# Kernel tuning notes

Measured on AMD Instinct MI355X. Metric: run time of the kernel, lower is better.

Reference implementation:

```python
import jax, jax.numpy as jnp
import numpy as np
import math
from jax import lax

B, T, GS = 16, 511, 1
OBS, OUT = 60, 30
D, H, L = 1024, 16, 8
DFF, HID = 4096, 100
S = T + GS
DH = D // H
EPS = 1e-5


def _ln(x, g, b):
    m = jnp.mean(x, axis=-1, keepdims=True)
    v = jnp.mean(jnp.square(x - m), axis=-1, keepdims=True)
    return (x - m) * lax.rsqrt(v + EPS) * g + b


def setup_inputs():
    key = jax.random.key(0)
    ks = iter(jax.random.split(key, 32))
    def n(shape):
        return jax.random.normal(next(ks), shape, dtype=jnp.float32) * 0.02
    return {
        "states": jax.random.normal(next(ks), (B, T, OBS), dtype=jnp.float32),
        "goals": jax.random.normal(next(ks), (B, GS, OBS), dtype=jnp.float32),
        "Wtok": n((OBS, D)), "btok": jnp.zeros((D,), jnp.float32),
        "pos": n((1, S, D)),
        "ln1_g": jnp.ones((L, D), jnp.float32), "ln1_b": jnp.zeros((L, D), jnp.float32),
        "Wq": n((L, D, D)), "bq": jnp.zeros((L, D), jnp.float32),
        "Wk": n((L, D, D)), "bk": jnp.zeros((L, D), jnp.float32),
        "Wv": n((L, D, D)), "bv": jnp.zeros((L, D), jnp.float32),
        "Wp": n((L, D, D)), "bp": jnp.zeros((L, D), jnp.float32),
        "ln2_g": jnp.ones((L, D), jnp.float32), "ln2_b": jnp.zeros((L, D), jnp.float32),
        "Wm1": n((L, D, DFF)), "bm1": jnp.zeros((L, DFF), jnp.float32),
        "Wm2": n((L, DFF, D)), "bm2": jnp.zeros((L, D), jnp.float32),
        "lnf_g": jnp.ones((D,), jnp.float32), "lnf_b": jnp.zeros((D,), jnp.float32),
        "Wh1": n((D, HID)), "bh1": jnp.zeros((HID,), jnp.float32),
        "Wh2": n((HID, OUT)), "bh2": jnp.zeros((OUT,), jnp.float32),
    }


def reference(states, goals, Wtok, btok, pos, ln1_g, ln1_b, Wq, bq, Wk, bk, Wv, bv, Wp, bp,
              ln2_g, ln2_b, Wm1, bm1, Wm2, bm2, lnf_g, lnf_b, Wh1, bh1, Wh2, bh2):
    # token + positional embeddings (dropout is identity in eval mode, pdrop=0)
    goal_x = goals @ Wtok + btok + pos[:, :GS]
    state_x = states @ Wtok + btok + pos[:, GS:S]
    x = jnp.concatenate([goal_x, state_x], axis=1)  # (B, S, D)
    mask = jnp.tril(jnp.ones((S, S), dtype=bool))
    scale = 1.0 / math.sqrt(DH)

    def block(x, p):
        g1, b1, wq, bq_, wk, bk_, wv, bv_, wp, bp_, g2, b2, w1, bm1_, w2, bm2_ = p
        h = _ln(x, g1, b1)
        q = (h @ wq + bq_).reshape(B, S, H, DH).transpose(0, 2, 1, 3)  # (B,H,S,DH)
        k = (h @ wk + bk_).reshape(B, S, H, DH).transpose(0, 2, 1, 3)
        v = (h @ wv + bv_).reshape(B, S, H, DH).transpose(0, 2, 1, 3)
        att = jnp.einsum('bhqd,bhkd->bhqk', q, k) * scale
        att = jnp.where(mask, att, -jnp.inf)
        att = jax.nn.softmax(att, axis=-1)
        y = jnp.einsum('bhqk,bhkd->bhqd', att, v)
        y = y.transpose(0, 2, 1, 3).reshape(B, S, D) @ wp + bp_
        x = x + y
        h = _ln(x, g2, b2)
        x = x + (jax.nn.gelu(h @ w1 + bm1_, approximate=False) @ w2 + bm2_)
        return x, None

    x, _ = lax.scan(block, x, (ln1_g, ln1_b, Wq, bq, Wk, bk, Wv, bv, Wp, bp,
                               ln2_g, ln2_b, Wm1, bm1, Wm2, bm2))
    x = _ln(x, lnf_g, lnf_b)[:, GS:]  # drop goal tokens -> (B, T, D)
    h = jax.nn.silu(x @ Wh1 + bh1)
    return h @ Wh2 + bh2
```

## Files before the change

kernel.cpp:

```cpp
#include <hip/hip_runtime.h>
#include <cstdint>
#include <math.h>

#define NB_B   16
#define NB_T   511
#define NB_S   512
#define NB_OBS 60
#define NB_D   1024
#define NB_H   16
#define NB_L   8
#define NB_DFF 4096
#define NB_HID 100
#define NB_OUT 30
#define NB_M   8192
#define QKV_S  3072

typedef __attribute__((ext_vector_type(8))) short  short8;
typedef __attribute__((ext_vector_type(4))) short  short4v;
typedef __attribute__((ext_vector_type(4))) float  f32x4;
typedef __attribute__((ext_vector_type(8))) __bf16 bf16x8;

template <int N_> struct ic { static constexpr int v = N_; };

__device__ __forceinline__ short f2bf(float f) {
  union { float f; unsigned u; } a; a.f = f;
  unsigned u = a.u + 0x7fffu + ((a.u >> 16) & 1u);
  return (short)(u >> 16);
}

__device__ __forceinline__ void load_lds16(const void* g, void* l) {
  __builtin_amdgcn_global_load_lds(
      (__attribute__((address_space(1))) unsigned int*)(uintptr_t)g,
      (__attribute__((address_space(3))) unsigned int*)(unsigned)(uintptr_t)l,
      16, 0, 0);
}

__device__ __forceinline__ f32x4 mfma16(short8 a, short8 b, f32x4 c) {
  return __builtin_amdgcn_mfma_f32_16x16x32_bf16(
      __builtin_bit_cast(bf16x8, a), __builtin_bit_cast(bf16x8, b), c, 0, 0, 0);
}

__device__ __forceinline__ float gelu_fast(float v) {
  const float t = 1.5957691216057308f * (v + 0.044715f * v * v * v);
  const float e = __expf(fminf(t, 30.f));
  return v * (e / (e + 1.f));
}

__global__ __launch_bounds__(256) void tconv2_kernel(
    const float* __restrict__ src, short* __restrict__ dst,
    int R, int C, size_t sstride, size_t dstride) {
  __shared__ float t[64][65];
  const float* s0 = src + blockIdx.z * sstride;
  short* d0 = dst + blockIdx.z * dstride;
  const int c0 = blockIdx.x * 64, r0 = blockIdx.y * 64;
#pragma unroll
  for (int i = 0; i < 4; i++) {
    const int idx = threadIdx.x + i * 256;
    const int r = idx >> 4, c4 = (idx & 15) * 4;
    const float4 v = *(const float4*)&s0[(size_t)(r0 + r) * C + c0 + c4];
    t[r][c4 + 0] = v.x; t[r][c4 + 1] = v.y; t[r][c4 + 2] = v.z; t[r][c4 + 3] = v.w;
  }
  __syncthreads();
#pragma unroll
  for (int i = 0; i < 2; i++) {
    const int idx = threadIdx.x + i * 256;
    const int c = idx >> 3, g = (idx & 7) * 8;
    short8 o;
#pragma unroll
    for (int j = 0; j < 8; j++) o[j] = f2bf(t[g + j][c]);
    *(short8*)&d0[(size_t)(c0 + c) * R + r0 + g] = o;
  }
}

__global__ __launch_bounds__(256) void whead_prep(
    const float* __restrict__ Wh1, const float* __restrict__ bh1,
    short* __restrict__ Wh1t, float* __restrict__ bh1p) {
  const int idx = blockIdx.x * 256 + threadIdx.x;
  const int n = idx >> 10, k = idx & 1023;
  Wh1t[idx] = (n < NB_HID) ? f2bf(Wh1[k * NB_HID + n]) : (short)0;
  if (idx < 128) bh1p[idx] = (idx < NB_HID) ? bh1[idx] : 0.f;
}

__global__ __launch_bounds__(256) void qkvbias_prep(
    const float* __restrict__ bq, const float* __restrict__ bk,
    const float* __restrict__ bv, float* __restrict__ outb) {
  const int idx = blockIdx.x * 256 + threadIdx.x;
  const int l = idx / QKV_S, r = idx - l * QKV_S;
  const int z = r >> 10, c = r & 1023;
  const float* src = (z == 0) ? bq : ((z == 1) ? bk : bv);
  outb[idx] = src[l * NB_D + c];
}

__global__ __launch_bounds__(256) void embed2_kernel(
    const float* __restrict__ states, const float* __restrict__ goals,
    const float* __restrict__ Wtok, const float* __restrict__ btok,
    const float* __restrict__ pos, float* __restrict__ x) {
  const int r0 = blockIdx.x * 8;
  __shared__ float tok[8][NB_OBS];
  for (int idx = threadIdx.x; idx < 8 * NB_OBS; idx += 256) {
    const int r = idx / NB_OBS, o = idx - r * NB_OBS;
    const int row = r0 + r, b = row >> 9, s = row & 511;
    tok[r][o] = (s == 0) ? goals[b * NB_OBS + o]
                         : states[((size_t)b * NB_T + (s - 1)) * NB_OBS + o];
  }
  __syncthreads();
#pragma unroll
  for (int i = 0; i < 4; i++) {
    const int d = threadIdx.x + i * 256;
    float acc[8];
#pragma unroll
    for (int r = 0; r < 8; r++) acc[r] = 0.f;
    for (int o = 0; o < NB_OBS; o++) {
      const float wv = Wtok[o * NB_D + d];
#pragma unroll
      for (int r = 0; r < 8; r++) acc[r] += tok[r][o] * wv;
    }
    const float bt = btok[d];
#pragma unroll
    for (int r = 0; r < 8; r++) {
      const int row = r0 + r, s = row & 511;
      x[(size_t)row * NB_D + d] = acc[r] + bt + pos[(size_t)s * NB_D + d];
    }
  }
}

template <typename OutT>
__global__ __launch_bounds__(256) void ln_wave(
    const float* __restrict__ xin, const float* __restrict__ gam,
    const float* __restrict__ bet, OutT* __restrict__ outp) {
  const int row = blockIdx.x * 4 + (threadIdx.x >> 6);
  const int lane = threadIdx.x & 63;
  const float4* src = (const float4*)(xin + (size_t)row * NB_D);
  float4 v[4];
  float s = 0.f, s2 = 0.f;
#pragma unroll
  for (int i = 0; i < 4; i++) {
    v[i] = src[lane + 64 * i];
    s += v[i].x + v[i].y + v[i].z + v[i].w;
    s2 += v[i].x * v[i].x + v[i].y * v[i].y + v[i].z * v[i].z + v[i].w * v[i].w;
  }
#pragma unroll
  for (int o = 32; o; o >>= 1) {
    s += __shfl_xor(s, o, 64);
    s2 += __shfl_xor(s2, o, 64);
  }
  const float mean = s * (1.f / NB_D);
  const float var = s2 * (1.f / NB_D) - mean * mean;
  const float rs = rsqrtf(var + 1e-5f);
#pragma unroll
  for (int i = 0; i < 4; i++) {
    const float4 g4 = ((const float4*)gam)[lane + 64 * i];
    const float4 b4 = ((const float4*)bet)[lane + 64 * i];
    const float o0 = (v[i].x - mean) * rs * g4.x + b4.x;
    const float o1 = (v[i].y - mean) * rs * g4.y + b4.y;
    const float o2 = (v[i].z - mean) * rs * g4.z + b4.z;
    const float o3 = (v[i].w - mean) * rs * g4.w + b4.w;
    if constexpr (sizeof(OutT) == 2) {
      short4v r = {f2bf(o0), f2bf(o1), f2bf(o2), f2bf(o3)};
      *(short4v*)((short*)outp + (size_t)row * NB_D + (lane + 64 * i) * 4) = r;
    } else {
      ((float4*)((float*)outp + (size_t)row * NB_D))[lane + 64 * i] =
          make_float4(o0, o1, o2, o3);
    }
  }
}

template <int ACT, bool RESID, typename OutT>
__global__ __launch_bounds__(256) void gemm_bt(
    const short* __restrict__ A, const short* __restrict__ Bt,
    const float* __restrict__ bias, const float* __restrict__ resid,
    OutT* __restrict__ C, int N, int K) {
  __shared__ short As[128][32];
  __shared__ short Bs[128][32];
  const int bm = blockIdx.y * 128, bn = blockIdx.x * 128;
  const int tid = threadIdx.x;
  const int w = tid >> 6, lane = tid & 63;
  const int wr = (w >> 1) * 64, wc = (w & 1) * 64;
  const int rr = lane & 15, sg = lane >> 4;

  f32x4 acc[4][4];
#pragma unroll
  for (int i = 0; i < 4; i++)
#pragma unroll
    for (int j = 0; j < 4; j++) acc[i][j] = f32x4{0.f, 0.f, 0.f, 0.f};

  const int srow0 = w * 32 + (lane >> 2);
  const int sslot = lane & 3;

  for (int k0 = 0; k0 < K; k0 += 32) {
    __syncthreads();
#pragma unroll
    for (int inst = 0; inst < 2; inst++) {
      const int r = srow0 + inst * 16;
      const int sl = sslot ^ ((r >> 1) & 3);
      load_lds16(A + (size_t)(bm + r) * K + k0 + sl * 8, &As[w * 32 + inst * 16][0]);
      load_lds16(Bt + (size_t)(bn + r) * K + k0 + sl * 8, &Bs[w * 32 + inst * 16][0]);
    }
    __syncthreads();
    short8 a[4], b[4];
#pragma unroll
    for (int i = 0; i < 4; i++) {
      const int r = wr + i * 16 + rr;
      a[i] = *(const short8*)&As[r][(sg ^ ((r >> 1) & 3)) * 8];
      const int c = wc + i * 16 + rr;
      b[i] = *(const short8*)&Bs[c][(sg ^ ((c >> 1) & 3)) * 8];
    }
#pragma unroll
    for (int i = 0; i < 4; i++)
#pragma unroll
      for (int j = 0; j < 4; j++) acc[i][j] = mfma16(a[i], b[j], acc[i][j]);
  }

#pragma unroll
  for (int j = 0; j < 4; j++) {
    const int col = bn + wc + j * 16 + rr;
    const float bv = bias[col];
#pragma unroll
    for (int i = 0; i < 4; i++) {
#pragma unroll
      for (int q = 0; q < 4; q++) {
        const int row = bm + wr + i * 16 + sg * 4 + q;
        float v = acc[i][j][q] + bv;
        if constexpr (RESID) v += resid[(size_t)row * N + col];
        if constexpr (ACT == 1) v = gelu_fast(v);
        if constexpr (ACT == 2) v = v / (1.f + __expf(-v));
        if constexpr (sizeof(OutT) == 2) C[(size_t)row * N + col] = (OutT)f2bf(v);
        else C[(size_t)row * N + col] = v;
      }
    }
  }
}

template <int BM, int N, int K, int ACT, bool RESID, typename OutT>
__device__ __forceinline__ void gemmv4_core(
    const short* __restrict__ A, const short* __restrict__ Bt,
    const float* __restrict__ bias, const float* __restrict__ resid,
    OutT* __restrict__ C) {
  constexpr int MI = BM / 32;
  constexpr int NK = K / 32;
  constexpr int NBN = N / 128;
  constexpr int NWG = (NB_M / BM) * NBN;
  constexpr int QC = NWG / 8;
  constexpr int L = 2 + BM / 64;
  constexpr int SA = BM * 32;

  __shared__ short As[3][SA];
  __shared__ short Bs[3][128 * 32];

  int wg = blockIdx.x;
  wg = (wg & 7) * QC + (wg >> 3);
  const int bm = (wg / NBN) * BM;
  const int bn = (wg % NBN) * 128;

  const int tid = threadIdx.x;
  const int w = tid >> 6, lane = tid & 63;
  const int wm = w >> 1, wn = w & 1;
  const int rr = lane & 15, sg = lane >> 4;
  const int lrow = lane >> 2, lslot = lane & 3;
  const int sslot = lslot ^ ((lrow >> 1) & 3);

  const short* Asrc = A + (size_t)(bm + w * 16 + lrow) * K + sslot * 8;
  const short* Bsrc = Bt + (size_t)(bn + w * 16 + lrow) * K + sslot * 8;
  short* Adst = &As[0][w * 512];
  short* Bdst = &Bs[0][w * 512];

  const int ar = wm * (BM / 2) + rr;
  const int br = wn * 64 + rr;
  const int aoff = ar * 32 + ((sg ^ ((ar >> 1) & 3)) * 8);
  const int boff = br * 32 + ((sg ^ ((br >> 1) & 3)) * 8);

  f32x4 acc[MI][4];
#pragma unroll
  for (int i = 0; i < MI; i++)
#pragma unroll
    for (int j = 0; j < 4; j++) acc[i][j] = f32x4{0.f, 0.f, 0.f, 0.f};

  auto stage = [&](int sb, int k0) {
    load_lds16(Bsrc + k0,                  Bdst + sb * 4096);
    load_lds16(Bsrc + (size_t)64 * K + k0, Bdst + sb * 4096 + 2048);
#pragma unroll
    for (int c = 0; c < BM / 64; c++)
      load_lds16(Asrc + (size_t)(c * 64) * K + k0, Adst + sb * SA + c * 2048);
  };

  auto gate = [&]() {
    if constexpr (L == 6) asm volatile("s_waitcnt vmcnt(6)" ::: "memory");
    else                  asm volatile("s_waitcnt vmcnt(4)" ::: "memory");
  };

  stage(0, 0);
  stage(1, 32);
  gate();
  __builtin_amdgcn_s_barrier();

  auto ktile = [&](auto BUFC, auto SBUFC, int t) {
    constexpr int BUF = decltype(BUFC)::v;
    constexpr int SBUF = decltype(SBUFC)::v;
    const short* Ab = &As[BUF][0];
    const short* Bb = &Bs[BUF][0];
    if (t + 2 < NK) stage(SBUF, (t + 2) * 32);
    short8 a[MI], b[4];
#pragma unroll
    for (int i = 0; i < MI; i++) a[i] = *(const short8*)(Ab + aoff + i * 512);
#pragma unroll
    for (int j = 0; j < 4; j++) b[j] = *(const short8*)(Bb + boff + j * 512);
    __builtin_amdgcn_s_setprio(1);
#pragma unroll
    for (int i = 0; i < MI; i++)
#pragma unroll
      for (int j = 0; j < 4; j++) acc[i][j] = mfma16(a[i], b[j], acc[i][j]);
    __builtin_amdgcn_s_setprio(0);
    if (t + 2 < NK)      gate();
    else if (t + 1 < NK) asm volatile("s_waitcnt vmcnt(0)" ::: "memory");
    __builtin_amdgcn_s_barrier();
  };

  int t = 0;
#pragma unroll 1
  for (; t + 3 <= NK; t += 3) {
    ktile(ic<0>{}, ic<2>{}, t);
    ktile(ic<1>{}, ic<0>{}, t + 1);
    ktile(ic<2>{}, ic<1>{}, t + 2);
  }
  if constexpr (NK % 3 >= 1) ktile(ic<0>{}, ic<2>{}, NK - NK % 3);
  if constexpr (NK % 3 >= 2) ktile(ic<1>{}, ic<0>{}, NK - NK % 3 + 1);

  const int col0 = bn + wn * 64 + rr;
  float bv[4];
#pragma unroll
  for (int j = 0; j < 4; j++) bv[j] = bias[col0 + j * 16];
#pragma unroll
  for (int i = 0; i < MI; i++) {
#pragma unroll
    for (int q = 0; q < 4; q++) {
      const size_t row = bm + wm * (BM / 2) + i * 16 + sg * 4 + q;
      float v0 = acc[i][0][q] + bv[0];
      float v1 = acc[i][1][q] + bv[1];
      float v2 = acc[i][2][q] + bv[2];
      float v3 = acc[i][3][q] + bv[3];
      if constexpr (RESID) {
        const float* rrow = resid + row * N + col0;
        v0 += rrow[0]; v1 += rrow[16]; v2 += rrow[32]; v3 += rrow[48];
      }
      if constexpr (ACT == 1) {
        v0 = gelu_fast(v0); v1 = gelu_fast(v1);
        v2 = gelu_fast(v2); v3 = gelu_fast(v3);
      }
      OutT* crow = C + row * N + col0;
      if constexpr (sizeof(OutT) == 2) {
        crow[0] = (OutT)f2bf(v0); crow[16] = (OutT)f2bf(v1);
        crow[32] = (OutT)f2bf(v2); crow[48] = (OutT)f2bf(v3);
      } else {
        crow[0] = v0; crow[16] = v1; crow[32] = v2; crow[48] = v3;
      }
    }
  }
}

template <int BM, int N, int K, int ACT, bool RESID, typename OutT>
__global__ __launch_bounds__(256, 2) void gemmv4(
    const short* __restrict__ A, const short* __restrict__ Bt,
    const float* __restrict__ bias, const float* __restrict__ resid,
    OutT* __restrict__ C) {
  gemmv4_core<BM, N, K, ACT, RESID, OutT>(A, Bt, bias, resid, C);
}

__global__ __launch_bounds__(256) void attn_kernel(
    const short* __restrict__ qkv, short* __restrict__ out) {
  const int qt = blockIdx.x, hh = blockIdx.y, bb = blockIdx.z;
  const int tid = threadIdx.x;
  const int w = tid >> 6, lane = tid & 63;
  const int rr = lane & 15, sg = lane >> 4;

  __shared__ short Ks[64][64];
  __shared__ short Vt[64][64];
  __shared__ short Ps[4][16][64];

  short8 qf[2];
  {
    const size_t qrow = (size_t)bb * NB_S + qt * 64 + w * 16 + rr;
#pragma unroll
    for (int ks = 0; ks < 2; ks++)
      qf[ks] = *(const short8*)&qkv[qrow * QKV_S + hh * 64 + ks * 32 + sg * 8];
  }

  float mrow[4], lrow[4];
  f32x4 o[4];
#pragma unroll
  for (int j = 0; j < 4; j++) { mrow[j] = -INFINITY; lrow[j] = 0.f; }
#pragma unroll
  for (int nb = 0; nb < 4; nb++) o[nb] = f32x4{0.f, 0.f, 0.f, 0.f};

  for (int kt = 0; kt <= qt; kt++) {
    __syncthreads();
    {
      const int p = lane & 7;
#pragma unroll
      for (int inst = 0; inst < 2; inst++) {
        const int r = w * 16 + inst * 8 + (lane >> 3);
        const int sl = p ^ (r & 7);
        load_lds16(qkv + ((size_t)bb * NB_S + kt * 64 + r) * QKV_S + 1024 + hh * 64 + sl * 8,
                   &Ks[w * 16 + inst * 8][0]);
      }
    }
    {
#pragma unroll
      for (int cc = 0; cc < 2; cc++) {
        const int c = tid * 2 + cc;
        const int sk = c >> 3, sl = c & 7;
        short8 vv = *(const short8*)&qkv[((size_t)bb * NB_S + kt * 64 + sk) * QKV_S + 2048 + hh * 64 + sl * 8];
        const int ss = sk >> 3;
#pragma unroll
        for (int j = 0; j < 8; j++) {
          const int dh = sl * 8 + j;
          Vt[dh][(ss ^ (dh & 7)) * 8 + (sk & 7)] = vv[j];
        }
      }
    }
    __syncthreads();

    f32x4 sf[4];
#pragma unroll
    for (int nb = 0; nb < 4; nb++) sf[nb] = f32x4{0.f, 0.f, 0.f, 0.f};
#pragma unroll
    for (int ks = 0; ks < 2; ks++) {
#pragma unroll
      for (int nb = 0; nb < 4; nb++) {
        const int ck = nb * 16 + rr;
        short8 kf = *(const short8*)&Ks[ck][((ks * 4 + sg) ^ (ck & 7)) * 8];
        sf[nb] = mfma16(qf[ks], kf, sf[nb]);
      }
    }
    const int rbase = qt * 64 + w * 16 + sg * 4;
    float pmax[4] = {-INFINITY, -INFINITY, -INFINITY, -INFINITY};
#pragma unroll
    for (int nb = 0; nb < 4; nb++) {
      const int cg = kt * 64 + nb * 16 + rr;
#pragma unroll
      for (int j = 0; j < 4; j++) {
        float sv = sf[nb][j] * 0.125f;
        if (cg > rbase + j) sv = -INFINITY;
        sf[nb][j] = sv;
        pmax[j] = fmaxf(pmax[j], sv);
      }
    }
#pragma unroll
    for (int o1 = 1; o1 < 16; o1 <<= 1)
#pragma unroll
      for (int j = 0; j < 4; j++)
        pmax[j] = fmaxf(pmax[j], __shfl_xor(pmax[j], o1, 64));

    float resc[4], psum[4];
#pragma unroll
    for (int j = 0; j < 4; j++) {
      const float mn = fmaxf(mrow[j], pmax[j]);
      resc[j] = __expf(mrow[j] - mn);
      mrow[j] = mn;
      psum[j] = 0.f;
    }
#pragma unroll
    for (int nb = 0; nb < 4; nb++)
#pragma unroll
      for (int j = 0; j < 4; j++) {
        const float p = __expf(sf[nb][j] - mrow[j]);
        sf[nb][j] = p;
        psum[j] += p;
      }
#pragma unroll
    for (int o1 = 1; o1 < 16; o1 <<= 1)
#pragma unroll
      for (int j = 0; j < 4; j++) psum[j] += __shfl_xor(psum[j], o1, 64);
#pragma unroll
    for (int j = 0; j < 4; j++) lrow[j] = lrow[j] * resc[j] + psum[j];
#pragma unroll
    for (int nb = 0; nb < 4; nb++)
#pragma unroll
      for (int j = 0; j < 4; j++) o[nb][j] *= resc[j];

#pragma unroll
    for (int nb = 0; nb < 4; nb++) {
      const int ck = nb * 16 + rr;
      const int ss = ck >> 3;
#pragma unroll
      for (int j = 0; j < 4; j++) {
        const int rq = sg * 4 + j;
        Ps[w][rq][(ss ^ (rq & 7)) * 8 + (ck & 7)] = f2bf(sf[nb][j]);
      }
    }
#pragma unroll
    for (int ks = 0; ks < 2; ks++) {
      short8 pf = *(const short8*)&Ps[w][rr][((ks * 4 + sg) ^ (rr & 7)) * 8];
#pragma unroll
      for (int nb = 0; nb < 4; nb++) {
        const int dh = nb * 16 + rr;
        short8 vf = *(const short8*)&Vt[dh][((ks * 4 + sg) ^ (dh & 7)) * 8];
        o[nb] = mfma16(pf, vf, o[nb]);
      }
    }
  }

  {
    const size_t orow0 = (size_t)bb * NB_S + qt * 64 + w * 16;
#pragma unroll
    for (int nb = 0; nb < 4; nb++)
#pragma unroll
      for (int j = 0; j < 4; j++) {
        const float v = o[nb][j] / lrow[j];
        out[(orow0 + sg * 4 + j) * NB_D + hh * 64 + nb * 16 + rr] = f2bf(v);
      }
  }
}

__global__ __launch_bounds__(256) void head2_kernel(
    const float* __restrict__ hbuf, const float* __restrict__ Wh2,
    const float* __restrict__ bh2, float* __restrict__ outp) {
  __shared__ float hs[8][NB_HID];
  const int g0 = blockIdx.x * 8;
  for (int idx = threadIdx.x; idx < 8 * NB_HID; idx += 256) {
    const int r = idx / NB_HID, k = idx - r * NB_HID;
    const int gt = g0 + r;
    const int b = gt / NB_T, tt = gt - b * NB_T;
    hs[r][k] = hbuf[(size_t)(b * NB_S + 1 + tt) * 128 + k];
  }
  __syncthreads();
  const int r = threadIdx.x >> 5, c = threadIdx.x & 31;
  if (c < NB_OUT) {
    float acc = bh2[c];
#pragma unroll
    for (int k = 0; k < NB_HID; k++) acc += hs[r][k] * Wh2[k * NB_OUT + c];
    outp[(size_t)(g0 + r) * NB_OUT + c] = acc;
  }
}

extern "C" void kernel_launch(void* const* d_in, const int* in_sizes, int n_in,
                              void* d_out, int out_size, void* d_ws, size_t ws_size,
                              hipStream_t stream) {
  const float* states = (const float*)d_in[0];
  const float* goals  = (const float*)d_in[1];
  const float* Wtok   = (const float*)d_in[2];
  const float* btok   = (const float*)d_in[3];
  const float* pos    = (const float*)d_in[4];
  const float* ln1_g  = (const float*)d_in[5];
  const float* ln1_b  = (const float*)d_in[6];
  const float* Wq     = (const float*)d_in[7];
  const float* bq     = (const float*)d_in[8];
  const float* Wk     = (const float*)d_in[9];
  const float* bk     = (const float*)d_in[10];
  const float* Wv     = (const float*)d_in[11];
  const float* bv     = (const float*)d_in[12];
  const float* Wp     = (const float*)d_in[13];
  const float* bp     = (const float*)d_in[14];
  const float* ln2_g  = (const float*)d_in[15];
  const float* ln2_b  = (const float*)d_in[16];
  const float* Wm1    = (const float*)d_in[17];
  const float* bm1    = (const float*)d_in[18];
  const float* Wm2    = (const float*)d_in[19];
  const float* bm2    = (const float*)d_in[20];
  const float* lnf_g  = (const float*)d_in[21];
  const float* lnf_b  = (const float*)d_in[22];
  const float* Wh1    = (const float*)d_in[23];
  const float* bh1    = (const float*)d_in[24];
  const float* Wh2    = (const float*)d_in[25];
  const float* bh2    = (const float*)d_in[26];

  char* wsp = (char*)d_ws;
  size_t off = 0;
  auto carve = [&](size_t bytes) -> char* {
    char* p = wsp + off;
    off += (bytes + 1023) & ~(size_t)1023;
    return p;
  };
  short* Wqkv_t = (short*)carve((size_t)NB_L * 3 * NB_D * NB_D * 2);
  short* Wp_t   = (short*)carve((size_t)NB_L * NB_D * NB_D * 2);
  short* Wm1_t  = (short*)carve((size_t)NB_L * NB_DFF * NB_D * 2);
  short* Wm2_t  = (short*)carve((size_t)NB_L * NB_D * NB_DFF * 2);
  float* x      = (float*)carve((size_t)NB_M * NB_D * 4);
  short* h      = (short*)carve((size_t)NB_M * NB_D * 2);
  short* qkvb   = (short*)carve((size_t)NB_M * QKV_S * 2);
  short* mlp    = (short*)carve((size_t)NB_M * NB_DFF * 2);
  short* Wh1t   = (short*)carve((size_t)128 * NB_D * 2);
  float* bh1p   = (float*)carve(128 * 4);
  float* bqkv   = (float*)carve((size_t)NB_L * QKV_S * 4);
  short* attout = mlp;
  float* hbuf   = (float*)qkvb;

  const dim3 thr(256);
  const size_t DD = (size_t)NB_D * NB_D;
  const size_t DF = (size_t)NB_D * NB_DFF;

  tconv2_kernel<<<dim3(16, 16, NB_L), thr, 0, stream>>>(Wq, Wqkv_t + 0 * DD, NB_D, NB_D, DD, 3 * DD);
  tconv2_kernel<<<dim3(16, 16, NB_L), thr, 0, stream>>>(Wk, Wqkv_t + 1 * DD, NB_D, NB_D, DD, 3 * DD);
  tconv2_kernel<<<dim3(16, 16, NB_L), thr, 0, stream>>>(Wv, Wqkv_t + 2 * DD, NB_D, NB_D, DD, 3 * DD);
  tconv2_kernel<<<dim3(16, 16, NB_L), thr, 0, stream>>>(Wp, Wp_t, NB_D, NB_D, DD, DD);
  tconv2_kernel<<<dim3(64, 16, NB_L), thr, 0, stream>>>(Wm1, Wm1_t, NB_D, NB_DFF, DF, DF);
  tconv2_kernel<<<dim3(16, 64, NB_L), thr, 0, stream>>>(Wm2, Wm2_t, NB_DFF, NB_D, DF, DF);
  whead_prep<<<512, thr, 0, stream>>>(Wh1, bh1, Wh1t, bh1p);
  qkvbias_prep<<<96, thr, 0, stream>>>(bq, bk, bv, bqkv);

  embed2_kernel<<<NB_M / 8, thr, 0, stream>>>(states, goals, Wtok, btok, pos, x);

  for (int l = 0; l < NB_L; l++) {
    ln_wave<short><<<NB_M / 4, thr, 0, stream>>>(x, ln1_g + l * NB_D, ln1_b + l * NB_D, h);
    gemmv4<256, QKV_S, NB_D, 0, false, short><<<768, thr, 0, stream>>>(
        h, Wqkv_t + (size_t)l * 3 * DD, bqkv + (size_t)l * QKV_S, nullptr, qkvb);
    attn_kernel<<<dim3(NB_S / 64, NB_H, NB_B), thr, 0, stream>>>(qkvb, attout);
    gemmv4<128, NB_D, NB_D, 0, true, float><<<512, thr, 0, stream>>>(
        attout, Wp_t + (size_t)l * DD, bp + l * NB_D, x, x);
    ln_wave<short><<<NB_M / 4, thr, 0, stream>>>(x, ln2_g + l * NB_D, ln2_b + l * NB_D, h);
    gemmv4<256, NB_DFF, NB_D, 1, false, short><<<1024, thr, 0, stream>>>(
        h, Wm1_t + (size_t)l * DF, bm1 + l * NB_DFF, nullptr, mlp);
    gemmv4<128, NB_D, NB_DFF, 0, true, float><<<512, thr, 0, stream>>>(
        mlp, Wm2_t + (size_t)l * DF, bm2 + l * NB_D, x, x);
  }

  ln_wave<short><<<NB_M / 4, thr, 0, stream>>>(x, lnf_g, lnf_b, h);
  gemm_bt<2, false, float><<<dim3(1, NB_M / 128), thr, 0, stream>>>(
      h, Wh1t, bh1p, nullptr, hbuf, 128, NB_D);
  head2_kernel<<<NB_M / 8, thr, 0, stream>>>(hbuf, Wh2, bh2, (float*)d_out);
}
```

Before: 2.872 ms.

## Add 256x256-tile 8-wave ping-pong GEMM for QKV and MLP-up projections

Introduces a new GEMM kernel with 512 threads (8 waves) computing 256x256 output tiles. It double-buffers K=64 slices in LDS, splits each tile into four MFMA quadrants interleaved with barriers and staggered async global-to-LDS loads, and raises wave priority during MFMA bursts. Workgroup IDs are remapped across 8 groups to improve L2 locality. The larger tile doubles operand reuse for the QKV and first MLP GEMMs, but uses 128KB of LDS and many barriers, which may limit occupancy.

```diff
diff --git a/kernel.cpp b/kernel.cpp
--- a/kernel.cpp
+++ b/kernel.cpp
@@ -363,6 +363,194 @@
     const float* __restrict__ bias, const float* __restrict__ resid,
     OutT* __restrict__ C) {
   gemmv4_core<BM, N, K, ACT, RESID, OutT>(A, Bt, bias, resid, C);
+}
+
+template <int N, int K, int ACT, typename OutT>
+__device__ __forceinline__ void gemm8p_core(
+    const short* __restrict__ A, const short* __restrict__ Bt,
+    const float* __restrict__ bias, OutT* __restrict__ C) {
+  constexpr int NK = K / 64;
+  constexpr int NBN = N / 256;
+  constexpr int NWG = (NB_M / 256) * NBN;
+  constexpr int QC = NWG / 8;
+  __shared__ short As[2][256 * 64];
+  __shared__ short Bs[2][256 * 64];
+
+  int wg = blockIdx.x;
+  wg = (wg & 7) * QC + (wg >> 3);
+  const int bm = (wg / NBN) * 256;
+  const int bn = (wg % NBN) * 256;
+
+  const int tid = threadIdx.x;
+  const int w = tid >> 6, lane = tid & 63;
+  const int wm = w >> 2, wn = w & 3;
+  const int rr = lane & 15, sg = lane >> 4;
+
+  const int srow = tid >> 3;
+  const int sslot = (tid & 7) ^ (srow & 7);
+  const short* srcA = A + (size_t)(bm + srow) * K + sslot * 8;
+  const short* srcB = Bt + (size_t)(bn + srow) * K + sslot * 8;
+  short* dstA = &As[0][w * 512];
+  short* dstB = &Bs[0][w * 512];
+
+  const int sw = rr & 7;
+  const int arow = wm * 128 + rr;
+  const int brow = wn * 64 + rr;
+  const int aoff0 = arow * 64 + ((0 + sg) ^ sw) * 8;
+  const int aoff1 = arow * 64 + ((4 + sg) ^ sw) * 8;
+  const int boff0 = brow * 64 + ((0 + sg) ^ sw) * 8;
+  const int boff1 = brow * 64 + ((4 + sg) ^ sw) * 8;
+
+  f32x4 acc[8][4];
+#pragma unroll
+  for (int i = 0; i < 8; i++)
+#pragma unroll
+    for (int j = 0; j < 4; j++) acc[i][j] = f32x4{0.f, 0.f, 0.f, 0.f};
+
+  auto stA = [&](int buf, int c, int tk) {
+    load_lds16(srcA + (size_t)(c * 64) * K + tk * 64,
+               dstA + buf * 16384 + c * 4096);
+  };
+  auto stB = [&](int buf, int c, int tk) {
+    load_lds16(srcB + (size_t)(c * 64) * K + tk * 64,
+               dstB + buf * 16384 + c * 4096);
+  };
+
+#pragma unroll
+  for (int c = 0; c < 4; c++) stA(0, c, 0);
+#pragma unroll
+  for (int c = 0; c < 4; c++) stB(0, c, 0);
+#pragma unroll
+  for (int c = 0; c < 4; c++) stA(1, c, 1);
+#pragma unroll
+  for (int c = 0; c < 4; c++) stB(1, c, 1);
+  asm volatile("s_waitcnt vmcnt(8)" ::: "memory");
+  __builtin_amdgcn_s_barrier();
+
+  auto tile = [&](auto BUFC, int t) {
+    constexpr int BUF = decltype(BUFC)::v;
+    const short* Ab = &As[BUF][0];
+    const short* Bb = &Bs[BUF][0];
+    const bool ds = (t + 2 < NK);
+    short8 aL[4][2], aH[4][2], bL[2][2], bH[2][2];
+
+#pragma unroll
+    for (int mi = 0; mi < 4; mi++) {
+      aL[mi][0] = *(const short8*)(Ab + aoff0 + mi * 1024);
+      aL[mi][1] = *(const short8*)(Ab + aoff1 + mi * 1024);
+    }
+#pragma unroll
+    for (int nj = 0; nj < 2; nj++) {
+      bL[nj][0] = *(const short8*)(Bb + boff0 + nj * 1024);
+      bL[nj][1] = *(const short8*)(Bb + boff1 + nj * 1024);
+    }
+    __builtin_amdgcn_s_barrier();
+    asm volatile("s_waitcnt lgkmcnt(0)" ::: "memory");
+    __builtin_amdgcn_s_setprio(1);
+#pragma unroll
+    for (int kk = 0; kk < 2; kk++)
+#pragma unroll
+      for (int mi = 0; mi < 4; mi++)
+#pragma unroll
+        for (int nj = 0; nj < 2; nj++)
+          acc[mi][nj] = mfma16(aL[mi][kk], bL[nj][kk], acc[mi][nj]);
+    __builtin_amdgcn_s_setprio(0);
+    __builtin_amdgcn_s_barrier();
+
+#pragma unroll
+    for (int nj = 0; nj < 2; nj++) {
+      bH[nj][0] = *(const short8*)(Bb + boff0 + (nj + 2) * 1024);
+      bH[nj][1] = *(const short8*)(Bb + boff1 + (nj + 2) * 1024);
+    }
+    if (ds) { stA(BUF, 0, t + 2); stA(BUF, 2, t + 2); }
+    __builtin_amdgcn_s_barrier();
+    asm volatile("s_waitcnt lgkmcnt(0)" ::: "memory");
+    __builtin_amdgcn_s_setprio(1);
+#pragma unroll
+    for (int kk = 0; kk < 2; kk++)
+#pragma unroll
+      for (int mi = 0; mi < 4; mi++)
+#pragma unroll
+        for (int nj = 0; nj < 2; nj++)
+          acc[mi][nj + 2] = mfma16(aL[mi][kk], bH[nj][kk], acc[mi][nj + 2]);
+    __builtin_amdgcn_s_setprio(0);
+    __builtin_amdgcn_s_barrier();
+
+#pragma unroll
+    for (int mi = 0; mi < 4; mi++) {
+      aH[mi][0] = *(const short8*)(Ab + aoff0 + (mi + 4) * 1024);
+      aH[mi][1] = *(const short8*)(Ab + aoff1 + (mi + 4) * 1024);
+    }
+    if (ds) { stB(BUF, 0, t + 2); stB(BUF, 1, t + 2); }
+    __builtin_amdgcn_s_barrier();
+    asm volatile("s_waitcnt lgkmcnt(0)" ::: "memory");
+    __builtin_amdgcn_s_setprio(1);
+#pragma unroll
+    for (int kk = 0; kk < 2; kk++)
+#pragma unroll
+      for (int mi = 0; mi < 4; mi++)
+#pragma unroll
+        for (int nj = 0; nj < 2; nj++)
+          acc[mi + 4][nj] = mfma16(aH[mi][kk], bL[nj][kk], acc[mi + 4][nj]);
+    __builtin_amdgcn_s_setprio(0);
+    __builtin_amdgcn_s_barrier();
+
+    if (ds) { stB(BUF, 2, t + 2); stB(BUF, 3, t + 2);
+              stA(BUF, 1, t + 2); stA(BUF, 3, t + 2); }
+    __builtin_amdgcn_s_barrier();
+    __builtin_amdgcn_s_setprio(1);
+#pragma unroll
+    for (int kk = 0; kk < 2; kk++)
+#pragma unroll
+      for (int mi = 0; mi < 4; mi++)
+#pragma unroll
+        for (int nj = 0; nj < 2; nj++)
+          acc[mi + 4][nj + 2] = mfma16(aH[mi][kk], bH[nj][kk], acc[mi + 4][nj + 2]);
+    __builtin_amdgcn_s_setprio(0);
+    if (ds)              asm volatile("s_waitcnt vmcnt(8)" ::: "memory");
+    else if (t + 1 < NK) asm volatile("s_waitcnt vmcnt(0)" ::: "memory");
+    __builtin_amdgcn_s_barrier();
+  };
+
+#pragma unroll 1
+  for (int t = 0; t < NK; t += 2) {
+    tile(ic<0>{}, t);
+    tile(ic<1>{}, t + 1);
+  }
+
+  const int col0 = bn + wn * 64 + rr;
+  float bv[4];
+#pragma unroll
+  for (int j = 0; j < 4; j++) bv[j] = bias[col0 + j * 16];
+#pragma unroll
+  for (int i = 0; i < 8; i++) {
+#pragma unroll
+    for (int q = 0; q < 4; q++) {
+      const size_t row = bm + wm * 128 + i * 16 + sg * 4 + q;
+      float v0 = acc[i][0][q] + bv[0];
+      float v1 = acc[i][1][q] + bv[1];
+      float v2 = acc[i][2][q] + bv[2];
+      float v3 = acc[i][3][q] + bv[3];
+      if constexpr (ACT == 1) {
+        v0 = gelu_fast(v0); v1 = gelu_fast(v1);
+        v2 = gelu_fast(v2); v3 = gelu_fast(v3);
+      }
+      OutT* crow = C + row * N + col0;
+      if constexpr (sizeof(OutT) == 2) {
+        crow[0] = (OutT)f2bf(v0); crow[16] = (OutT)f2bf(v1);
+        crow[32] = (OutT)f2bf(v2); crow[48] = (OutT)f2bf(v3);
+      } else {
+        crow[0] = v0; crow[16] = v1; crow[32] = v2; crow[48] = v3;
+      }
+    }
+  }
+}
+
+template <int N, int K, int ACT, typename OutT>
+__global__ __launch_bounds__(512, 2) void gemm8p(
+    const short* __restrict__ A, const short* __restrict__ Bt,
+    const float* __restrict__ bias, OutT* __restrict__ C) {
+  gemm8p_core<N, K, ACT, OutT>(A, Bt, bias, C);
 }
 
 __global__ __launch_bounds__(256) void attn_kernel(
@@ -584,7 +772,7 @@
   short* attout = mlp;
   float* hbuf   = (float*)qkvb;
 
-  const dim3 thr(256);
+  const dim3 thr(256), thr8(512);
   const size_t DD = (size_t)NB_D * NB_D;
   const size_t DF = (size_t)NB_D * NB_DFF;
 
@@ -601,14 +789,14 @@
 
   for (int l = 0; l < NB_L; l++) {
     ln_wave<short><<<NB_M / 4, thr, 0, stream>>>(x, ln1_g + l * NB_D, ln1_b + l * NB_D, h);
-    gemmv4<256, QKV_S, NB_D, 0, false, short><<<768, thr, 0, stream>>>(
-        h, Wqkv_t + (size_t)l * 3 * DD, bqkv + (size_t)l * QKV_S, nullptr, qkvb);
+    gemm8p<QKV_S, NB_D, 0, short><<<384, thr8, 0, stream>>>(
+        h, Wqkv_t + (size_t)l * 3 * DD, bqkv + (size_t)l * QKV_S, qkvb);
     attn_kernel<<<dim3(NB_S / 64, NB_H, NB_B), thr, 0, stream>>>(qkvb, attout);
     gemmv4<128, NB_D, NB_D, 0, true, float><<<512, thr, 0, stream>>>(
         attout, Wp_t + (size_t)l * DD, bp + l * NB_D, x, x);
     ln_wave<short><<<NB_M / 4, thr, 0, stream>>>(x, ln2_g + l * NB_D, ln2_b + l * NB_D, h);
-    gemmv4<256, NB_DFF, NB_D, 1, false, short><<<1024, thr, 0, stream>>>(
-        h, Wm1_t + (size_t)l * DF, bm1 + l * NB_DFF, nullptr, mlp);
+    gemm8p<NB_DFF, NB_D, 1, short><<<512, thr8, 0, stream>>>(
+        h, Wm1_t + (size_t)l * DF, bm1 + l * NB_DFF, mlp);
     gemmv4<128, NB_D, NB_DFF, 0, true, float><<<512, thr, 0, stream>>>(
         mlp, Wm2_t + (size_t)l * DF, bm2 + l * NB_D, x, x);
   }
```

After: 2.968 ms. 3.3% more time.

## Replace triple-buffered GEMM with simple single-buffer 128x128 tile kernel

Applied to the files above, without the earlier changes.

Swaps the triple-buffered, vmcnt-gated gemmv4 kernel (BM 256/128) for a simpler gemmv5 that uses a fixed 128x128 tile, one LDS buffer, and two __syncthreads per k-step. Occupancy rises to 4 workgroups per CU, so the intent is to hide latency through more resident waves rather than software pipelining. The trade-off is that global-to-LDS loads no longer overlap with MFMA inside a workgroup, and the larger-M tiles used for the QKV and MLP1 GEMMs, with their extra reuse, are gone.

```diff
diff --git a/kernel.cpp b/kernel.cpp
--- a/kernel.cpp
+++ b/kernel.cpp
@@ -19,8 +19,6 @@
 typedef __attribute__((ext_vector_type(4))) short  short4v;
 typedef __attribute__((ext_vector_type(4))) float  f32x4;
 typedef __attribute__((ext_vector_type(8))) __bf16 bf16x8;
-
-template <int N_> struct ic { static constexpr int v = N_; };
 
 __device__ __forceinline__ short f2bf(float f) {
   union { float f; unsigned u; } a; a.f = f;
@@ -165,6 +163,99 @@
   }
 }
 
+template <int N, int K, int ACT, bool RESID, typename OutT>
+__global__ __launch_bounds__(256, 4) void gemmv5(
+    const short* __restrict__ A, const short* __restrict__ Bt,
+    const float* __restrict__ bias, const float* __restrict__ resid,
+    OutT* __restrict__ C) {
+  constexpr int NBN = N / 128;
+  constexpr int NWG = (NB_M / 128) * NBN;
+  constexpr int QC = NWG / 8;
+  __shared__ short As[128][32];
+  __shared__ short Bs[128][32];
+
+  int wg = blockIdx.x;
+  wg = (wg & 7) * QC + (wg >> 3);
+  const int bm = (wg / NBN) * 128;
+  const int bn = (wg % NBN) * 128;
+
+  const int tid = threadIdx.x;
+  const int w = tid >> 6, lane = tid & 63;
+  const int wr = (w >> 1) * 64, wc = (w & 1) * 64;
+  const int rr = lane & 15, sg = lane >> 4;
+
+  f32x4 acc[4][4];
+#pragma unroll
+  for (int i = 0; i < 4; i++)
+#pragma unroll
+    for (int j = 0; j < 4; j++) acc[i][j] = f32x4{0.f, 0.f, 0.f, 0.f};
+
+  const int srow0 = w * 32 + (lane >> 2);
+  const int sslot = lane & 3;
+  const int sl0 = sslot ^ ((srow0 >> 1) & 3);
+  const int sl1 = sslot ^ (((srow0 + 16) >> 1) & 3);
+  const short* Asrc0 = A + (size_t)(bm + srow0) * K + sl0 * 8;
+  const short* Asrc1 = A + (size_t)(bm + srow0 + 16) * K + sl1 * 8;
+  const short* Bsrc0 = Bt + (size_t)(bn + srow0) * K + sl0 * 8;
+  const short* Bsrc1 = Bt + (size_t)(bn + srow0 + 16) * K + sl1 * 8;
+
+  const int ar = wr + rr, bcr = wc + rr;
+  const int aoff = ar * 32 + (sg ^ ((ar >> 1) & 3)) * 8;
+  const int boff = bcr * 32 + (sg ^ ((bcr >> 1) & 3)) * 8;
+
+  for (int k0 = 0; k0 < K; k0 += 32) {
+    __syncthreads();
+    load_lds16(Asrc0 + k0, &As[w * 32][0]);
+    load_lds16(Asrc1 + k0, &As[w * 32 + 16][0]);
+    load_lds16(Bsrc0 + k0, &Bs[w * 32][0]);
+    load_lds16(Bsrc1 + k0, &Bs[w * 32 + 16][0]);
+    __syncthreads();
+    short8 a[4], b[4];
+#pragma unroll
+    for (int i = 0; i < 4; i++) {
+      a[i] = *(const short8*)((const short*)As + aoff + i * 512);
+      b[i] = *(const short8*)((const short*)Bs + boff + i * 512);
+    }
+    __builtin_amdgcn_s_setprio(1);
+#pragma unroll
+    for (int i = 0; i < 4; i++)
+#pragma unroll
+      for (int j = 0; j < 4; j++) acc[i][j] = mfma16(a[i], b[j], acc[i][j]);
+    __builtin_amdgcn_s_setprio(0);
+  }
+
+  const int col0 = bn + wc + rr;
+  float bv[4];
+#pragma unroll
+  for (int j = 0; j < 4; j++) bv[j] = bias[col0 + j * 16];
+#pragma unroll
+  for (int i = 0; i < 4; i++) {
+#pragma unroll
+    for (int q = 0; q < 4; q++) {
+      const size_t row = bm + wr + i * 16 + sg * 4 + q;
+      float v0 = acc[i][0][q] + bv[0];
+      float v1 = acc[i][1][q] + bv[1];
+      float v2 = acc[i][2][q] + bv[2];
+      float v3 = acc[i][3][q] + bv[3];
+      if constexpr (RESID) {
+        const float* rrow = resid + row * N + col0;
+        v0 += rrow[0]; v1 += rrow[16]; v2 += rrow[32]; v3 += rrow[48];
+      }
+      if constexpr (ACT == 1) {
+        v0 = gelu_fast(v0); v1 = gelu_fast(v1);
+        v2 = gelu_fast(v2); v3 = gelu_fast(v3);
+      }
+      OutT* crow = C + row * N + col0;
+      if constexpr (sizeof(OutT) == 2) {
+        crow[0] = (OutT)f2bf(v0); crow[16] = (OutT)f2bf(v1);
+        crow[32] = (OutT)f2bf(v2); crow[48] = (OutT)f2bf(v3);
+      } else {
+        crow[0] = v0; crow[16] = v1; crow[32] = v2; crow[48] = v3;
+      }
+    }
+  }
+}
+
 template <int ACT, bool RESID, typename OutT>
 __global__ __launch_bounds__(256) void gemm_bt(
     const short* __restrict__ A, const short* __restrict__ Bt,
@@ -229,140 +320,6 @@
       }
     }
   }
-}
-
-template <int BM, int N, int K, int ACT, bool RESID, typename OutT>
-__device__ __forceinline__ void gemmv4_core(
-    const short* __restrict__ A, const short* __restrict__ Bt,
-    const float* __restrict__ bias, const float* __restrict__ resid,
-    OutT* __restrict__ C) {
-  constexpr int MI = BM / 32;
-  constexpr int NK = K / 32;
-  constexpr int NBN = N / 128;
-  constexpr int NWG = (NB_M / BM) * NBN;
-  constexpr int QC = NWG / 8;
-  constexpr int L = 2 + BM / 64;
-  constexpr int SA = BM * 32;
-
-  __shared__ short As[3][SA];
-  __shared__ short Bs[3][128 * 32];
-
-  int wg = blockIdx.x;
-  wg = (wg & 7) * QC + (wg >> 3);
-  const int bm = (wg / NBN) * BM;
-  const int bn = (wg % NBN) * 128;
-
-  const int tid = threadIdx.x;
-  const int w = tid >> 6, lane = tid & 63;
-  const int wm = w >> 1, wn = w & 1;
-  const int rr = lane & 15, sg = lane >> 4;
-  const int lrow = lane >> 2, lslot = lane & 3;
-  const int sslot = lslot ^ ((lrow >> 1) & 3);
-
-  const short* Asrc = A + (size_t)(bm + w * 16 + lrow) * K + sslot * 8;
-  const short* Bsrc = Bt + (size_t)(bn + w * 16 + lrow) * K + sslot * 8;
-  short* Adst = &As[0][w * 512];
-  short* Bdst = &Bs[0][w * 512];
-
-  const int ar = wm * (BM / 2) + rr;
-  const int br = wn * 64 + rr;
-  const int aoff = ar * 32 + ((sg ^ ((ar >> 1) & 3)) * 8);
-  const int boff = br * 32 + ((sg ^ ((br >> 1) & 3)) * 8);
-
-  f32x4 acc[MI][4];
-#pragma unroll
-  for (int i = 0; i < MI; i++)
-#pragma unroll
-    for (int j = 0; j < 4; j++) acc[i][j] = f32x4{0.f, 0.f, 0.f, 0.f};
-
-  auto stage = [&](int sb, int k0) {
-    load_lds16(Bsrc + k0,                  Bdst + sb * 4096);
-    load_lds16(Bsrc + (size_t)64 * K + k0, Bdst + sb * 4096 + 2048);
-#pragma unroll
-    for (int c = 0; c < BM / 64; c++)
-      load_lds16(Asrc + (size_t)(c * 64) * K + k0, Adst + sb * SA + c * 2048);
-  };
-
-  auto gate = [&]() {
-    if constexpr (L == 6) asm volatile("s_waitcnt vmcnt(6)" ::: "memory");
-    else                  asm volatile("s_waitcnt vmcnt(4)" ::: "memory");
-  };
-
-  stage(0, 0);
-  stage(1, 32);
-  gate();
-  __builtin_amdgcn_s_barrier();
-
-  auto ktile = [&](auto BUFC, auto SBUFC, int t) {
-    constexpr int BUF = decltype(BUFC)::v;
-    constexpr int SBUF = decltype(SBUFC)::v;
-    const short* Ab = &As[BUF][0];
-    const short* Bb = &Bs[BUF][0];
-    if (t + 2 < NK) stage(SBUF, (t + 2) * 32);
-    short8 a[MI], b[4];
-#pragma unroll
-    for (int i = 0; i < MI; i++) a[i] = *(const short8*)(Ab + aoff + i * 512);
-#pragma unroll
-    for (int j = 0; j < 4; j++) b[j] = *(const short8*)(Bb + boff + j * 512);
-    __builtin_amdgcn_s_setprio(1);
-#pragma unroll
-    for (int i = 0; i < MI; i++)
-#pragma unroll
-      for (int j = 0; j < 4; j++) acc[i][j] = mfma16(a[i], b[j], acc[i][j]);
-    __builtin_amdgcn_s_setprio(0);
-    if (t + 2 < NK)      gate();
-    else if (t + 1 < NK) asm volatile("s_waitcnt vmcnt(0)" ::: "memory");
-    __builtin_amdgcn_s_barrier();
-  };
-
-  int t = 0;
-#pragma unroll 1
-  for (; t + 3 <= NK; t += 3) {
-    ktile(ic<0>{}, ic<2>{}, t);
-    ktile(ic<1>{}, ic<0>{}, t + 1);
-    ktile(ic<2>{}, ic<1>{}, t + 2);
-  }
-  if constexpr (NK % 3 >= 1) ktile(ic<0>{}, ic<2>{}, NK - NK % 3);
-  if constexpr (NK % 3 >= 2) ktile(ic<1>{}, ic<0>{}, NK - NK % 3 + 1);
-
-  const int col0 = bn + wn * 64 + rr;
-  float bv[4];
-#pragma unroll
-  for (int j = 0; j < 4; j++) bv[j] = bias[col0 + j * 16];
-#pragma unroll
-  for (int i = 0; i < MI; i++) {
-#pragma unroll
-    for (int q = 0; q < 4; q++) {
-      const size_t row = bm + wm * (BM / 2) + i * 16 + sg * 4 + q;
-      float v0 = acc[i][0][q] + bv[0];
-      float v1 = acc[i][1][q] + bv[1];
-      float v2 = acc[i][2][q] + bv[2];
-      float v3 = acc[i][3][q] + bv[3];
-      if constexpr (RESID) {
-        const float* rrow = resid + row * N + col0;
-        v0 += rrow[0]; v1 += rrow[16]; v2 += rrow[32]; v3 += rrow[48];
-      }
-      if constexpr (ACT == 1) {
-        v0 = gelu_fast(v0); v1 = gelu_fast(v1);
-        v2 = gelu_fast(v2); v3 = gelu_fast(v3);
-      }
-      OutT* crow = C + row * N + col0;
-      if constexpr (sizeof(OutT) == 2) {
-        crow[0] = (OutT)f2bf(v0); crow[16] = (OutT)f2bf(v1);
-        crow[32] = (OutT)f2bf(v2); crow[48] = (OutT)f2bf(v3);
-      } else {
-        crow[0] = v0; crow[16] = v1; crow[32] = v2; crow[48] = v3;
-      }
-    }
-  }
-}
-
-template <int BM, int N, int K, int ACT, bool RESID, typename OutT>
-__global__ __launch_bounds__(256, 2) void gemmv4(
-    const short* __restrict__ A, const short* __restrict__ Bt,
-    const float* __restrict__ bias, const float* __restrict__ resid,
-    OutT* __restrict__ C) {
-  gemmv4_core<BM, N, K, ACT, RESID, OutT>(A, Bt, bias, resid, C);
 }
 
 __global__ __launch_bounds__(256) void attn_kernel(
@@ -601,15 +558,15 @@
 
   for (int l = 0; l < NB_L; l++) {
     ln_wave<short><<<NB_M / 4, thr, 0, stream>>>(x, ln1_g + l * NB_D, ln1_b + l * NB_D, h);
-    gemmv4<256, QKV_S, NB_D, 0, false, short><<<768, thr, 0, stream>>>(
+    gemmv5<QKV_S, NB_D, 0, false, short><<<1536, thr, 0, stream>>>(
         h, Wqkv_t + (size_t)l * 3 * DD, bqkv + (size_t)l * QKV_S, nullptr, qkvb);
     attn_kernel<<<dim3(NB_S / 64, NB_H, NB_B), thr, 0, stream>>>(qkvb, attout);
-    gemmv4<128, NB_D, NB_D, 0, true, float><<<512, thr, 0, stream>>>(
+    gemmv5<NB_D, NB_D, 0, true, float><<<512, thr, 0, stream>>>(
         attout, Wp_t + (size_t)l * DD, bp + l * NB_D, x, x);
     ln_wave<short><<<NB_M / 4, thr, 0, stream>>>(x, ln2_g + l * NB_D, ln2_b + l * NB_D, h);
-    gemmv4<256, NB_DFF, NB_D, 1, false, short><<<1024, thr, 0, stream>>>(
+    gemmv5<NB_DFF, NB_D, 1, false, short><<<2048, thr, 0, stream>>>(
         h, Wm1_t + (size_t)l * DF, bm1 + l * NB_DFF, nullptr, mlp);
-    gemmv4<128, NB_D, NB_DFF, 0, true, float><<<512, thr, 0, stream>>>(
+    gemmv5<NB_D, NB_DFF, 0, true, float><<<512, thr, 0, stream>>>(
         mlp, Wm2_t + (size_t)l * DF, bm2 + l * NB_D, x, x);
   }
 
```

After: 3.174 ms. 10.5% more time.
